# Performance work log

Measured on AMD Instinct MI355X. Metric: run time of the kernel, lower is better.

## Reference

```python
import jax, jax.numpy as jnp
import numpy as np

T, B, S = 8, 4, 2048
LAT, SYM, NC = 1024, 256, 512


def setup_inputs() -> dict:
    key = jax.random.key(0)
    ks = jax.random.split(key, 16)
    inp = {
        "token_state": jax.random.normal(ks[0], (B, S, LAT), jnp.float32),
        "bus_symbols": jax.random.normal(ks[1], (T, B, S, SYM), jnp.float32),
        "bus_indices": jax.random.randint(ks[2], (T, B, S), 0, NC),
        "bus_outputs": jax.random.normal(ks[3], (T, B, S, LAT), jnp.float32),
        "bus_mask": jnp.zeros((T,), jnp.bool_),
        # parameters (stored as (in, out) matrices)
        "Wq": jax.random.normal(ks[4], (SYM, 1), jnp.float32) / np.sqrt(SYM),
        "bq": jnp.zeros((1,), jnp.float32),
        "Wread": jax.random.normal(ks[5], (2 * LAT, LAT), jnp.float32) / np.sqrt(2 * LAT),
        "bread": jnp.zeros((LAT,), jnp.float32),
        "Wsym": jax.random.normal(ks[6], (LAT, SYM), jnp.float32) / np.sqrt(LAT),
        "bsym": jnp.zeros((SYM,), jnp.float32),
        "Wc1": jax.random.normal(ks[7], (LAT + SYM, LAT), jnp.float32) / np.sqrt(LAT + SYM),
        "bc1": jnp.zeros((LAT,), jnp.float32),
        "Wc2": jax.random.normal(ks[8], (LAT, LAT), jnp.float32) / np.sqrt(LAT),
        "bc2": jnp.zeros((LAT,), jnp.float32),
        "codebook": jax.random.normal(ks[9], (NC, SYM), jnp.float32),
    }
    return inp


def reference(token_state, bus_symbols, bus_indices, bus_outputs, bus_mask,
              Wq, bq, Wread, bread, Wsym, bsym, Wc1, bc1, Wc2, bc2, codebook):
    Tm, Bb, Ss, Dsym = bus_symbols.shape
    N = Bb * Ss
    syms = bus_symbols.reshape(Tm, N, Dsym)          # [T, N, SYM]
    outs = bus_outputs.reshape(Tm, N, -1)            # [T, N, LAT]

    # top-1 bus message routing
    relevance = (syms @ Wq + bq)[..., 0]             # [T, N]
    top_msg_idx = jnp.argmax(relevance, axis=0)      # [N]
    chosen = jnp.take_along_axis(outs, top_msg_idx[None, :, None], axis=0)[0]  # [N, LAT]
    bus_context = chosen.reshape(Bb, Ss, -1)

    z = jnp.concatenate([token_state, bus_context], axis=-1)
    z_read = z @ Wread + bread                       # [B, S, LAT]
    raw_symbol = z_read @ Wsym + bsym                # [B, S, SYM]

    # VQ: cdist argmin (squared distance has same argmin)
    flat = raw_symbol.reshape(-1, Dsym)              # [N, SYM]
    d2 = (jnp.sum(flat * flat, axis=1, keepdims=True)
          - 2.0 * flat @ codebook.T
          + jnp.sum(codebook * codebook, axis=1)[None, :])  # [N, NC]
    indices = jnp.argmin(d2, axis=-1)                # [N]
    quantized = codebook[indices].reshape(Bb, Ss, Dsym)

    h = jax.nn.relu(jnp.concatenate([z_read, quantized], axis=-1) @ Wc1 + bc1)
    node_output = h @ Wc2 + bc2 + token_state

    used_counts = jnp.zeros((Tm,), jnp.int32).at[top_msg_idx].add(1)
    keep_mask = used_counts == 0
    return node_output, quantized, indices.reshape(Bb, Ss), keep_mask
```

## Files before the change

### kernel.cpp

```cpp
#include <hip/hip_runtime.h>
#include <hip/hip_bf16.h>

#define DEVI __device__ __forceinline__

namespace {

constexpr int T_   = 8;
constexpr int NTOK = 8192;
constexpr int LAT  = 1024;
constexpr int SYM  = 256;
constexpr int NC   = 512;
constexpr float TAU = 0.6f;

typedef short short8 __attribute__((ext_vector_type(8)));
typedef float floatx4 __attribute__((ext_vector_type(4)));

DEVI unsigned short f2bf(float f){
  union { float f; unsigned u; } v; v.f = f;
  return (unsigned short)((v.u + 0x7fffu + ((v.u >> 16) & 1u)) >> 16);
}

DEVI void gload_lds16(const void* g, void* l){
  __builtin_amdgcn_global_load_lds((const __attribute__((address_space(1))) void*)g,
                                   (__attribute__((address_space(3))) void*)l, 16, 0, 0);
}

__global__ void routepack_k(const float* __restrict__ syms, const float* __restrict__ Wq,
                            const float* __restrict__ ts, const float* __restrict__ bus,
                            int* __restrict__ top, int* __restrict__ counts,
                            unsigned short* __restrict__ Az){
  int gt = blockIdx.x * blockDim.x + threadIdx.x;
  int wid = gt >> 6, lane = gt & 63;
  float4 wq = *(const float4*)(Wq + lane * 4);
  float best = -INFINITY; int bt = 0;
  for (int t = 0; t < T_; ++t){
    float4 s = *(const float4*)(syms + ((size_t)t * NTOK + wid) * SYM + lane * 4);
    float p = s.x*wq.x + s.y*wq.y + s.z*wq.z + s.w*wq.w;
    #pragma unroll
    for (int off = 32; off; off >>= 1) p += __shfl_down(p, off, 64);
    p = __shfl(p, 0, 64);
    if (p > best){ best = p; bt = t; }
  }
  if (lane == 0){ top[wid] = bt; atomicAdd(&counts[bt], 1); }
  const float* tsrow  = ts  + (size_t)wid * LAT;
  const float* busrow = bus + ((size_t)bt * NTOK + wid) * LAT;
  unsigned short* az  = Az + (size_t)wid * (2*LAT);
  #pragma unroll
  for (int i = 0; i < 4; ++i){
    int c = (i*64 + lane) * 4;
    float4 v = *(const float4*)(tsrow + c);
    ushort4 o; o.x = f2bf(v.x); o.y = f2bf(v.y); o.z = f2bf(v.z); o.w = f2bf(v.w);
    *(ushort4*)(az + c) = o;
    float4 w = *(const float4*)(busrow + c);
    ushort4 p2; p2.x = f2bf(w.x); p2.y = f2bf(w.y); p2.z = f2bf(w.z); p2.w = f2bf(w.w);
    *(ushort4*)(az + LAT + c) = p2;
  }
}

constexpr int MP_WFUSE = 128, MP_WCOMB = 384, MP_T32 = 4736, MP_CNORM = 4864;

DEVI void dev_wfuse(int tb, int tid, float* smem,
                    const float* __restrict__ Wsym, const float* __restrict__ cb,
                    unsigned short* __restrict__ WfuseT){
  float (*As)[68] = (float(*)[68])smem;
  float (*Bs)[68] = (float(*)[68])(smem + 544);
  const int bxm = tb & 15, byn = tb >> 4;
  const int m0 = bxm * 64, n0 = byn * 64;
  const int tx = tid & 15, ty = tid >> 4;
  float acc[4][4] = {};
  for (int k0 = 0; k0 < SYM; k0 += 8){
    if (tid < 128){
      int m = tid >> 1, kq = (tid & 1) * 4;
      float4 v = *(const float4*)(Wsym + (size_t)(m0+m) * SYM + k0 + kq);
      As[kq+0][m] = v.x; As[kq+1][m] = v.y; As[kq+2][m] = v.z; As[kq+3][m] = v.w;
    }
    {
      int n = tid >> 2, kk = (tid & 3) * 2;
      float2 v = *(const float2*)(cb + (size_t)(n0+n) * SYM + k0 + kk);
      Bs[kk+0][n] = v.x; Bs[kk+1][n] = v.y;
    }
    __syncthreads();
    #pragma unroll
    for (int k = 0; k < 8; ++k){
      float a[4], b[4];
      #pragma unroll
      for (int i = 0; i < 4; ++i) a[i] = As[k][ty*4 + i];
      #pragma unroll
      for (int j = 0; j < 4; ++j) b[j] = Bs[k][tx*4 + j];
      #pragma unroll
      for (int i = 0; i < 4; ++i)
        #pragma unroll
        for (int j = 0; j < 4; ++j) acc[i][j] += a[i] * b[j];
    }
    __syncthreads();
  }
  #pragma unroll
  for (int i = 0; i < 4; ++i)
    #pragma unroll
    for (int j = 0; j < 4; ++j)
      WfuseT[(size_t)(n0 + tx*4 + j) * LAT + m0 + ty*4 + i] = f2bf(acc[i][j]);
}

DEVI void dev_wcomb(int tb, int tid, float* smem,
                    const float* __restrict__ Wread, const float* __restrict__ Wsym,
                    float* __restrict__ Wcomb){
  float (*As)[68] = (float(*)[68])smem;
  float (*Bs)[68] = (float(*)[68])(smem + 544);
  const int bxm = tb & 63, byn = tb >> 6;
  const int m0 = bxm * 32, n0 = byn * 64;
  const int tx = tid & 15, ty = tid >> 4;
  float acc[2][4] = {};
  for (int k0 = 0; k0 < LAT; k0 += 8){
    if (tid < 64){
      int m = tid >> 1, kq = (tid & 1) * 4;
      float4 v = *(const float4*)(Wread + (size_t)(m0+m) * LAT + k0 + kq);
      As[kq+0][m] = v.x; As[kq+1][m] = v.y; As[kq+2][m] = v.z; As[kq+3][m] = v.w;
    }
    if (tid < 128){
      int k = tid >> 4, n4 = (tid & 15) * 4;
      *(float4*)&Bs[k][n4] = *(const float4*)(Wsym + (size_t)(k0+k) * SYM + n0 + n4);
    }
    __syncthreads();
    #pragma unroll
    for (int k = 0; k < 8; ++k){
      float a[2], b[4];
      #pragma unroll
      for (int i = 0; i < 2; ++i) a[i] = As[k][ty*2 + i];
      #pragma unroll
      for (int j = 0; j < 4; ++j) b[j] = Bs[k][tx*4 + j];
      #pragma unroll
      for (int i = 0; i < 2; ++i)
        #pragma unroll
        for (int j = 0; j < 4; ++j) acc[i][j] += a[i] * b[j];
    }
    __syncthreads();
  }
  #pragma unroll
  for (int i = 0; i < 2; ++i)
    #pragma unroll
    for (int j = 0; j < 4; ++j)
      Wcomb[(size_t)(m0 + ty*2 + i) * SYM + n0 + tx*4 + j] = acc[i][j];
}

DEVI void dev_t32(int t, int tid, float* smem,
                  const float* __restrict__ in, unsigned short* __restrict__ out,
                  int R, int C){
  float (*tile)[33] = (float(*)[33])smem;
  int bx = t % 32, by = t / 32;
  int r0 = by * 32, c0 = bx * 32;
  int tx = tid & 31, ty = tid >> 5;
  #pragma unroll
  for (int j = 0; j < 4; ++j)
    tile[ty + j*8][tx] = in[(size_t)(r0 + ty + j*8) * C + c0 + tx];
  __syncthreads();
  #pragma unroll
  for (int j = 0; j < 4; ++j)
    out[(size_t)(c0 + ty + j*8) * R + r0 + tx] = f2bf(tile[tx][ty + j*8]);
}

DEVI void dev_cnorm(int lb, int tid, const float* __restrict__ cb,
                    const float* __restrict__ bsym,
                    float* __restrict__ cnorm, float* __restrict__ svec){
  int wid = lb * 4 + (tid >> 6), lane = tid & 63;
  float4 v = *(const float4*)(cb + (size_t)wid * SYM + lane * 4);
  float4 b = *(const float4*)(bsym + lane * 4);
  float p = v.x*v.x + v.y*v.y + v.z*v.z + v.w*v.w;
  float q = v.x*(v.x-2.f*b.x) + v.y*(v.y-2.f*b.y) + v.z*(v.z-2.f*b.z) + v.w*(v.w-2.f*b.w);
  #pragma unroll
  for (int off = 32; off; off >>= 1){ p += __shfl_down(p, off, 64); q += __shfl_down(q, off, 64); }
  if (lane == 0){ cnorm[wid] = p; svec[wid] = q; }
}

DEVI void dev_rbias(int tid, const float* __restrict__ bread,
                    const float* __restrict__ Wsym, const float* __restrict__ bsym,
                    float* __restrict__ rb){
  float a0=0.f,a1=0.f,a2=0.f,a3=0.f;
  for (int k = 0; k < LAT; k += 4){
    a0 += bread[k+0] * Wsym[(size_t)(k+0) * SYM + tid];
    a1 += bread[k+1] * Wsym[(size_t)(k+1) * SYM + tid];
    a2 += bread[k+2] * Wsym[(size_t)(k+2) * SYM + tid];
    a3 += bread[k+3] * Wsym[(size_t)(k+3) * SYM + tid];
  }
  rb[tid] = bsym[tid] + ((a0+a1)+(a2+a3));
}

__global__ __launch_bounds__(256)
void megaprep_k(const float* __restrict__ Wsym, const float* __restrict__ cb,
                unsigned short* __restrict__ WfuseT,
                const float* __restrict__ Wread, float* __restrict__ Wcomb,
                unsigned short* __restrict__ WreadT,
                const float* __restrict__ Wc1, unsigned short* __restrict__ Wc1T,
                const float* __restrict__ Wc2, unsigned short* __restrict__ Wc2T,
                const float* __restrict__ bsym, float* __restrict__ cnorm,
                float* __restrict__ svec,
                const float* __restrict__ bread, float* __restrict__ rb){
  __shared__ float smem[1088];
  int b = blockIdx.x, tid = threadIdx.x;
  if (b < MP_WFUSE){
    dev_wfuse(b, tid, smem, Wsym, cb, WfuseT);
  } else if (b < MP_WCOMB){
    dev_wcomb(b - MP_WFUSE, tid, smem, Wread, Wsym, Wcomb);
  } else if (b < MP_T32){
    int t = b - MP_WCOMB;
    if (t < 2048)      dev_t32(t,        tid, smem, Wread, WreadT, 2*LAT, LAT);
    else if (t < 3328) dev_t32(t - 2048, tid, smem, Wc1,   Wc1T,   LAT+SYM, LAT);
    else               dev_t32(t - 3328, tid, smem, Wc2,   Wc2T,   LAT,  LAT);
  } else if (b < MP_CNORM){
    dev_cnorm(b - MP_T32, tid, cb, bsym, cnorm, svec);
  } else {
    dev_rbias(tid, bread, Wsym, bsym, rb);
  }
}

constexpr int A_PLAIN = 0, A_CAT = 1;
constexpr int EP_ZH = 0, EP_VQ = 1, EP_RELU = 2, EP_OUT = 3;

template<int ASRC, int EPI>
__global__ __launch_bounds__(256)
void mgemm(const unsigned short* __restrict__ A, const unsigned short* __restrict__ A2,
           const unsigned short* __restrict__ BT, const float* __restrict__ bias,
           const float* __restrict__ resid,
           unsigned short* __restrict__ Cb, float* __restrict__ Cf,
           int N, int K, int asplit)
{
  __shared__ unsigned short As[128*32];
  __shared__ unsigned short Bs[128*32];
  const int tid  = threadIdx.x;
  const int wave = tid >> 6, lane = tid & 63;
  const int wy = wave >> 1, wx = wave & 1;
  const int lq = lane >> 4, lr = lane & 15;

  const int nwg  = gridDim.x * gridDim.y;
  const int orig = blockIdx.y * gridDim.x + blockIdx.x;
  const int dec  = (orig & 7) * (nwg >> 3) + (orig >> 3);
  const int bx   = dec % gridDim.x, by = dec / gridDim.x;
  const int m0 = by * 128, n0 = bx * 128;

  floatx4 acc[4][4] = {};

  for (int k0 = 0; k0 < K; k0 += 32){
    #pragma unroll
    for (int c = 0; c < 2; ++c){
      int chunk = tid + c*256;
      int mrel = chunk >> 2, kc = (chunk & 3) * 8;
      int gk = k0 + kc;
      const unsigned short* srcA;
      if constexpr (ASRC == A_CAT){
        if (gk < asplit) srcA = A  + (size_t)(m0+mrel) * asplit + gk;
        else             srcA = A2 + (size_t)(m0+mrel) * (K-asplit) + (gk-asplit);
      } else {
        srcA = A + (size_t)(m0+mrel) * K + gk;
      }
      gload_lds16(srcA, &As[(c*256 + wave*64) * 8]);
      gload_lds16(BT + (size_t)(n0+mrel) * K + gk, &Bs[(c*256 + wave*64) * 8]);
    }
    __syncthreads();
    short8 af[4], bf[4];
    #pragma unroll
    for (int i = 0; i < 4; ++i){
      af[i] = *(const short8*)&As[(wy*64 + i*16 + lr)*32 + lq*8];
      bf[i] = *(const short8*)&Bs[(wx*64 + i*16 + lr)*32 + lq*8];
    }
    #pragma unroll
    for (int i = 0; i < 4; ++i)
      #pragma unroll
      for (int j = 0; j < 4; ++j)
        acc[i][j] = __builtin_amdgcn_mfma_f32_16x16x32_bf16(af[i], bf[j], acc[i][j], 0, 0, 0);
    __syncthreads();
  }

  #pragma unroll
  for (int i = 0; i < 4; ++i){
    #pragma unroll
    for (int j = 0; j < 4; ++j){
      int gn = n0 + wx*64 + j*16 + lr;
      #pragma unroll
      for (int r = 0; r < 4; ++r){
        int gm = m0 + wy*64 + i*16 + lq*4 + r;
        float v = acc[i][j][r];
        if constexpr (EPI == EP_ZH){
          Cb[(size_t)gm * N + gn] = f2bf(v + bias[gn]);
        } else if constexpr (EPI == EP_VQ){
          Cf[(size_t)gm * N + gn] = bias[gn] - 2.f * v;
        } else if constexpr (EPI == EP_RELU){
          float u = v + bias[gn];
          Cb[(size_t)gm * N + gn] = f2bf(u > 0.f ? u : 0.f);
        } else {
          Cf[(size_t)gm * N + gn] = v + bias[gn] + resid[(size_t)gm * N + gn];
        }
      }
    }
  }
}

__global__ void vq_k(const float* __restrict__ scores, const float* __restrict__ cb,
                     float* __restrict__ out_q, float* __restrict__ out_idx,
                     unsigned short* __restrict__ q_h,
                     int* __restrict__ rcount, int* __restrict__ rlist,
                     const int* __restrict__ counts, float* __restrict__ out_mask){
  if (blockIdx.x == 0 && threadIdx.x < T_)
    out_mask[threadIdx.x] = (counts[threadIdx.x] == 0) ? 1.0f : 0.0f;
  int gt = blockIdx.x * blockDim.x + threadIdx.x;
  int wid = gt >> 6, lane = gt & 63;
  if (wid >= NTOK) return;
  const float* row = scores + (size_t)wid * NC;
  float v1 = INFINITY, v2 = INFINITY; int i1 = 0x7fffffff;
  #pragma unroll
  for (int i = 0; i < NC/64; ++i){
    int c = i*64 + lane;
    float v = row[c];
    if (v < v1){ v2 = v1; v1 = v; i1 = c; } else v2 = fminf(v2, v);
  }
  #pragma unroll
  for (int off = 32; off; off >>= 1){
    float ov1 = __shfl_down(v1, off, 64);
    int   oi1 = __shfl_down(i1, off, 64);
    float ov2 = __shfl_down(v2, off, 64);
    float rest;
    if (ov1 < v1 || (ov1 == v1 && oi1 < i1)){ rest = v1; v1 = ov1; i1 = oi1; }
    else rest = ov1;
    v2 = fminf(fminf(v2, ov2), rest);
  }
  i1 = __shfl(i1, 0, 64);
  if (lane == 0){
    out_idx[wid] = (float)i1;
    if (__shfl(v2, 0, 64) - __shfl(v1, 0, 64) < TAU){
      int p = atomicAdd(rcount, 1); rlist[p] = wid;
    }
  }
  float4 cv = *(const float4*)(cb + (size_t)i1 * SYM + lane * 4);
  *(float4*)(out_q + (size_t)wid * SYM + lane * 4) = cv;
  ushort4 qh; qh.x = f2bf(cv.x); qh.y = f2bf(cv.y); qh.z = f2bf(cv.z); qh.w = f2bf(cv.w);
  *(ushort4*)(q_h + (size_t)wid * SYM + lane * 4) = qh;
}

constexpr int RT = 4;

__global__ __launch_bounds__(256)
void repair_k(const int* __restrict__ rcount, const int* __restrict__ rlist,
              const int* __restrict__ top,
              const float* __restrict__ ts, const float* __restrict__ bus,
              const float* __restrict__ Wcomb, const float* __restrict__ rb,
              const float* __restrict__ cb, const float* __restrict__ cnorm,
              float* __restrict__ out_q, float* __restrict__ out_idx,
              unsigned short* __restrict__ q_h){
  __shared__ float a[RT][2*LAT];
  __shared__ float raw[RT][SYM];
  __shared__ float pv[RT][4];
  __shared__ int   pi[RT][4];
  __shared__ int   fidx[RT];
  int tid = threadIdx.x;
  int lane = tid & 63, wave = tid >> 6;
  int cnt = *rcount;
  int nchunk = (cnt + RT - 1) / RT;
  for (int ch = blockIdx.x; ch < nchunk; ch += gridDim.x){
    int base = ch * RT;
    int nt = min(RT, cnt - base);
    for (int q = tid; q < nt * 512; q += 256){
      int t = q >> 9, c = (q & 511) * 4;
      int m = rlist[base + t];
      int tp = top[m];
      float4 v = (c < LAT) ? *(const float4*)(ts + (size_t)m * LAT + c)
                           : *(const float4*)(bus + ((size_t)tp * NTOK + m) * LAT + (c - LAT));
      *(float4*)&a[t][c] = v;
    }
    __syncthreads();
    float acc0[RT], acc1[RT], acc2[RT], acc3[RT];
    #pragma unroll
    for (int t = 0; t < RT; ++t){ acc0[t]=0.f; acc1[t]=0.f; acc2[t]=0.f; acc3[t]=0.f; }
    for (int k = 0; k < 2*LAT; k += 4){
      float w0 = Wcomb[(size_t)(k+0) * SYM + tid];
      float w1 = Wcomb[(size_t)(k+1) * SYM + tid];
      float w2 = Wcomb[(size_t)(k+2) * SYM + tid];
      float w3 = Wcomb[(size_t)(k+3) * SYM + tid];
      #pragma unroll
      for (int t = 0; t < RT; ++t){
        float4 av = *(const float4*)&a[t][k];
        acc0[t] += av.x * w0; acc1[t] += av.y * w1;
        acc2[t] += av.z * w2; acc3[t] += av.w * w3;
      }
    }
    #pragma unroll
    for (int t = 0; t < RT; ++t)
      raw[t][tid] = rb[tid] + ((acc0[t] + acc1[t]) + (acc2[t] + acc3[t]));
    __syncthreads();
    float bv[RT]; int bi[RT];
    #pragma unroll
    for (int t = 0; t < RT; ++t){ bv[t] = INFINITY; bi[t] = 0x7fffffff; }
    #pragma unroll
    for (int cc = 0; cc < 2; ++cc){
      int c = tid + cc * 256;
      const float* cr = cb + (size_t)c * SYM;
      float d[RT] = {};
      for (int j = 0; j < SYM; j += 4){
        float4 cv = *(const float4*)(cr + j);
        #pragma unroll
        for (int t = 0; t < RT; ++t){
          float4 rv4 = *(const float4*)&raw[t][j];
          d[t] += rv4.x*cv.x + rv4.y*cv.y + rv4.z*cv.z + rv4.w*cv.w;
        }
      }
      #pragma unroll
      for (int t = 0; t < RT; ++t){
        float s = cnorm[c] - 2.f * d[t];
        if (s < bv[t] || (s == bv[t] && c < bi[t])){ bv[t] = s; bi[t] = c; }
      }
    }
    #pragma unroll
    for (int t = 0; t < RT; ++t){
      float v = bv[t]; int i = bi[t];
      #pragma unroll
      for (int off = 32; off; off >>= 1){
        float ov = __shfl_down(v, off, 64);
        int   oi = __shfl_down(i, off, 64);
        if (ov < v || (ov == v && oi < i)){ v = ov; i = oi; }
      }
      if (lane == 0){ pv[t][wave] = v; pi[t][wave] = i; }
    }
    __syncthreads();
    if (tid < nt){
      float v = pv[tid][0]; int i = pi[tid][0];
      #pragma unroll
      for (int w = 1; w < 4; ++w){
        if (pv[tid][w] < v || (pv[tid][w] == v && pi[tid][w] < i)){ v = pv[tid][w]; i = pi[tid][w]; }
      }
      fidx[tid] = i;
      out_idx[rlist[base + tid]] = (float)i;
    }
    __syncthreads();
    for (int t = 0; t < nt; ++t){
      int m = rlist[base + t];
      int idx = fidx[t];
      float cvv = cb[(size_t)idx * SYM + tid];
      out_q[(size_t)m * SYM + tid] = cvv;
      q_h[(size_t)m * SYM + tid] = f2bf(cvv);
    }
    __syncthreads();
  }
}

}

extern "C" void kernel_launch(void* const* d_in, const int* in_sizes, int n_in,
                              void* d_out, int out_size, void* d_ws, size_t ws_size,
                              hipStream_t stream){
  const float* token_state = (const float*)d_in[0];
  const float* bus_symbols = (const float*)d_in[1];
  const float* bus_outputs = (const float*)d_in[3];
  const float* Wq    = (const float*)d_in[5];
  const float* Wread = (const float*)d_in[7];
  const float* bread = (const float*)d_in[8];
  const float* Wsym  = (const float*)d_in[9];
  const float* bsym  = (const float*)d_in[10];
  const float* Wc1   = (const float*)d_in[11];
  const float* bc1   = (const float*)d_in[12];
  const float* Wc2   = (const float*)d_in[13];
  const float* bc2   = (const float*)d_in[14];
  const float* codebook = (const float*)d_in[15];

  float* out_node = (float*)d_out;
  float* out_quant= out_node + (size_t)NTOK * LAT;
  float* out_idx  = out_quant + (size_t)NTOK * SYM;
  float* out_mask = out_idx + NTOK;

  char* W = (char*)d_ws; size_t off = 0;
  auto alloc = [&](size_t bytes)->char*{ char* p = W + off; off = (off + bytes + 255) & ~(size_t)255; return p; };
  int*   top     = (int*)alloc(NTOK*4);
  char*  zeroed  = alloc(256);
  int*   counts  = (int*)zeroed;
  int*   rcount  = (int*)(zeroed + 128);
  int*   rlist   = (int*)alloc(NTOK*4);
  float* cnorm   = (float*)alloc(NC*4);
  float* svec    = (float*)alloc(NC*4);
  float* rb      = (float*)alloc(SYM*4);
  float* Wcomb   = (float*)alloc((size_t)2*LAT*SYM*4);
  unsigned short* WreadT = (unsigned short*)alloc((size_t)LAT*2*LAT*2);
  unsigned short* Wc1T   = (unsigned short*)alloc((size_t)LAT*(LAT+SYM)*2);
  unsigned short* Wc2T   = (unsigned short*)alloc((size_t)LAT*LAT*2);
  unsigned short* WfuseT = (unsigned short*)alloc((size_t)NC*LAT*2);
  unsigned short* z_h    = (unsigned short*)alloc((size_t)NTOK*LAT*2);
  unsigned short* q_h    = (unsigned short*)alloc((size_t)NTOK*SYM*2);
  unsigned short* h_h    = (unsigned short*)alloc((size_t)NTOK*LAT*2);
  char* az_region        = alloc((size_t)NTOK*2*LAT*2);
  unsigned short* A_z    = (unsigned short*)az_region;
  float* scores          = (float*)az_region;

  hipMemsetAsync(zeroed, 0, 256, stream);

  routepack_k<<<NTOK/4, 256, 0, stream>>>(bus_symbols, Wq, token_state, bus_outputs,
                                          top, counts, A_z);
  megaprep_k<<<MP_CNORM + 1, 256, 0, stream>>>(
      Wsym, codebook, WfuseT, Wread, Wcomb, WreadT, Wc1, Wc1T, Wc2, Wc2T,
      bsym, cnorm, svec, bread, rb);

  mgemm<A_PLAIN, EP_ZH><<<dim3(LAT/128, NTOK/128), 256, 0, stream>>>(
      A_z, nullptr, WreadT, bread, nullptr, z_h, nullptr, LAT, 2*LAT, 0);
  mgemm<A_PLAIN, EP_VQ><<<dim3(NC/128, NTOK/128), 256, 0, stream>>>(
      z_h, nullptr, WfuseT, svec, nullptr, nullptr, scores, NC, LAT, 0);

  vq_k<<<NTOK/4, 256, 0, stream>>>(scores, codebook, out_quant, out_idx, q_h,
                                   rcount, rlist, counts, out_mask);
  repair_k<<<512, 256, 0, stream>>>(rcount, rlist, top, token_state, bus_outputs,
                                    Wcomb, rb, codebook, cnorm, out_quant, out_idx, q_h);

  mgemm<A_CAT, EP_RELU><<<dim3(LAT/128, NTOK/128), 256, 0, stream>>>(
      z_h, q_h, Wc1T, bc1, nullptr, h_h, nullptr, LAT, LAT+SYM, LAT);
  mgemm<A_PLAIN, EP_OUT><<<dim3(LAT/128, NTOK/128), 256, 0, stream>>>(
      h_h, nullptr, Wc2T, bc2, token_state, nullptr, out_node, LAT, LAT, 0);
}
```

Baseline: 797.9 us.

## Fuse VQ score GEMM with argmin and codebook gather into one kernel

Replaces the separate score GEMM, which wrote an fp32 NTOK x NC score matrix, and the vq_k argmin kernel with a single kernel. Each block computes 64 token rows against all 512 codewords and keeps top-2 values in registers, then gathers the chosen codewords. The per-token atomic count for the keep mask is replaced by a presence bitmask built in block 0, and the memset is replaced by zeroing rcount inside routepack_k. This removes the score matrix round trip and two launches, but the grid shrinks to 128 blocks with a 64-row tile, which may underfill the GPU, and block 0 carries extra mask work.

```diff
diff --git a/kernel.cpp b/kernel.cpp
--- a/kernel.cpp
+++ b/kernel.cpp
@@ -27,8 +27,9 @@
 
 __global__ void routepack_k(const float* __restrict__ syms, const float* __restrict__ Wq,
                             const float* __restrict__ ts, const float* __restrict__ bus,
-                            int* __restrict__ top, int* __restrict__ counts,
+                            int* __restrict__ top, int* __restrict__ rcount,
                             unsigned short* __restrict__ Az){
+  if (blockIdx.x == 0 && threadIdx.x == 0) *rcount = 0;
   int gt = blockIdx.x * blockDim.x + threadIdx.x;
   int wid = gt >> 6, lane = gt & 63;
   float4 wq = *(const float4*)(Wq + lane * 4);
@@ -41,7 +42,7 @@
     p = __shfl(p, 0, 64);
     if (p > best){ best = p; bt = t; }
   }
-  if (lane == 0){ top[wid] = bt; atomicAdd(&counts[bt], 1); }
+  if (lane == 0) top[wid] = bt;
   const float* tsrow  = ts  + (size_t)wid * LAT;
   const float* busrow = bus + ((size_t)bt * NTOK + wid) * LAT;
   unsigned short* az  = Az + (size_t)wid * (2*LAT);
@@ -213,7 +214,7 @@
 }
 
 constexpr int A_PLAIN = 0, A_CAT = 1;
-constexpr int EP_ZH = 0, EP_VQ = 1, EP_RELU = 2, EP_OUT = 3;
+constexpr int EP_ZH = 0, EP_RELU = 2, EP_OUT = 3;
 
 template<int ASRC, int EPI>
 __global__ __launch_bounds__(256)
@@ -280,8 +281,6 @@
         float v = acc[i][j][r];
         if constexpr (EPI == EP_ZH){
           Cb[(size_t)gm * N + gn] = f2bf(v + bias[gn]);
-        } else if constexpr (EPI == EP_VQ){
-          Cf[(size_t)gm * N + gn] = bias[gn] - 2.f * v;
         } else if constexpr (EPI == EP_RELU){
           float u = v + bias[gn];
           Cb[(size_t)gm * N + gn] = f2bf(u > 0.f ? u : 0.f);
@@ -293,45 +292,132 @@
   }
 }
 
-__global__ void vq_k(const float* __restrict__ scores, const float* __restrict__ cb,
-                     float* __restrict__ out_q, float* __restrict__ out_idx,
-                     unsigned short* __restrict__ q_h,
-                     int* __restrict__ rcount, int* __restrict__ rlist,
-                     const int* __restrict__ counts, float* __restrict__ out_mask){
-  if (blockIdx.x == 0 && threadIdx.x < T_)
-    out_mask[threadIdx.x] = (counts[threadIdx.x] == 0) ? 1.0f : 0.0f;
-  int gt = blockIdx.x * blockDim.x + threadIdx.x;
-  int wid = gt >> 6, lane = gt & 63;
-  if (wid >= NTOK) return;
-  const float* row = scores + (size_t)wid * NC;
-  float v1 = INFINITY, v2 = INFINITY; int i1 = 0x7fffffff;
-  #pragma unroll
-  for (int i = 0; i < NC/64; ++i){
-    int c = i*64 + lane;
-    float v = row[c];
-    if (v < v1){ v2 = v1; v1 = v; i1 = c; } else v2 = fminf(v2, v);
-  }
-  #pragma unroll
-  for (int off = 32; off; off >>= 1){
-    float ov1 = __shfl_down(v1, off, 64);
-    int   oi1 = __shfl_down(i1, off, 64);
-    float ov2 = __shfl_down(v2, off, 64);
-    float rest;
-    if (ov1 < v1 || (ov1 == v1 && oi1 < i1)){ rest = v1; v1 = ov1; i1 = oi1; }
-    else rest = ov1;
-    v2 = fminf(fminf(v2, ov2), rest);
-  }
-  i1 = __shfl(i1, 0, 64);
-  if (lane == 0){
-    out_idx[wid] = (float)i1;
-    if (__shfl(v2, 0, 64) - __shfl(v1, 0, 64) < TAU){
-      int p = atomicAdd(rcount, 1); rlist[p] = wid;
-    }
-  }
-  float4 cv = *(const float4*)(cb + (size_t)i1 * SYM + lane * 4);
-  *(float4*)(out_q + (size_t)wid * SYM + lane * 4) = cv;
-  ushort4 qh; qh.x = f2bf(cv.x); qh.y = f2bf(cv.y); qh.z = f2bf(cv.z); qh.w = f2bf(cv.w);
-  *(ushort4*)(q_h + (size_t)wid * SYM + lane * 4) = qh;
+__global__ __launch_bounds__(256)
+void vqgemm_k(const unsigned short* __restrict__ A ,
+              const unsigned short* __restrict__ BT ,
+              const float* __restrict__ svec, const float* __restrict__ cb,
+              const int* __restrict__ top,
+              float* __restrict__ out_q, float* __restrict__ out_idx,
+              unsigned short* __restrict__ q_h,
+              int* __restrict__ rcount, int* __restrict__ rlist,
+              float* __restrict__ out_mask)
+{
+  __shared__ unsigned short As[64*32];
+  __shared__ unsigned short Bs[128*32];
+  __shared__ float red_v1[64][2]; __shared__ int red_i1[64][2]; __shared__ float red_v2[64][2];
+  __shared__ int ridx[64];
+  __shared__ int presw[4];
+  const int tid = threadIdx.x;
+  const int wave = tid >> 6, lane = tid & 63;
+  const int wy = wave >> 1, wx = wave & 1;
+  const int lq = lane >> 4, lr = lane & 15;
+  const int nwg = gridDim.x;
+  const int orig = blockIdx.x;
+  const int blk = (orig & 7) * (nwg >> 3) + (orig >> 3);
+  const int m0 = blk * 64;
+
+  if (orig == 0){
+    int pres = 0;
+    for (int i = tid; i < NTOK; i += 256) pres |= 1 << top[i];
+    #pragma unroll
+    for (int off = 32; off; off >>= 1) pres |= __shfl_down(pres, off, 64);
+    if (lane == 0) presw[wave] = pres;
+    __syncthreads();
+    if (tid < T_){
+      int all = presw[0] | presw[1] | presw[2] | presw[3];
+      out_mask[tid] = ((all >> tid) & 1) ? 0.0f : 1.0f;
+    }
+    __syncthreads();
+  }
+
+  float t1v[8], t2v[8]; int t1i[8];
+  #pragma unroll
+  for (int q = 0; q < 8; ++q){ t1v[q] = INFINITY; t2v[q] = INFINITY; t1i[q] = 0x7fffffff; }
+
+  for (int nc = 0; nc < 4; ++nc){
+    const int n0c = nc * 128;
+    floatx4 acc[2][4] = {};
+    for (int k0 = 0; k0 < LAT; k0 += 32){
+      {
+        int mrel = tid >> 2, kc = (tid & 3) * 8;
+        gload_lds16(A + (size_t)(m0+mrel) * LAT + k0 + kc, &As[(wave*64) * 8]);
+      }
+      #pragma unroll
+      for (int c = 0; c < 2; ++c){
+        int chunk = tid + c*256;
+        int mrel = chunk >> 2, kc = (chunk & 3) * 8;
+        gload_lds16(BT + (size_t)(n0c+mrel) * LAT + k0 + kc, &Bs[(c*256 + wave*64) * 8]);
+      }
+      __syncthreads();
+      short8 af[2], bf[4];
+      #pragma unroll
+      for (int i = 0; i < 2; ++i)
+        af[i] = *(const short8*)&As[(wy*32 + i*16 + lr)*32 + lq*8];
+      #pragma unroll
+      for (int j = 0; j < 4; ++j)
+        bf[j] = *(const short8*)&Bs[(wx*64 + j*16 + lr)*32 + lq*8];
+      #pragma unroll
+      for (int i = 0; i < 2; ++i)
+        #pragma unroll
+        for (int j = 0; j < 4; ++j)
+          acc[i][j] = __builtin_amdgcn_mfma_f32_16x16x32_bf16(af[i], bf[j], acc[i][j], 0, 0, 0);
+      __syncthreads();
+    }
+    #pragma unroll
+    for (int j = 0; j < 4; ++j){
+      int col = n0c + wx*64 + j*16 + lr;
+      float sv = svec[col];
+      #pragma unroll
+      for (int i = 0; i < 2; ++i){
+        #pragma unroll
+        for (int r = 0; r < 4; ++r){
+          int q = i*4 + r;
+          float s = sv - 2.f * acc[i][j][r];
+          if (s < t1v[q]){ t2v[q] = t1v[q]; t1v[q] = s; t1i[q] = col; }
+          else t2v[q] = fminf(t2v[q], s);
+        }
+      }
+    }
+  }
+
+  #pragma unroll
+  for (int q = 0; q < 8; ++q){
+    float v1 = t1v[q]; int i1 = t1i[q]; float v2 = t2v[q];
+    #pragma unroll
+    for (int m = 8; m; m >>= 1){
+      float ov1 = __shfl_xor(v1, m, 64);
+      int   oi1 = __shfl_xor(i1, m, 64);
+      float ov2 = __shfl_xor(v2, m, 64);
+      if (ov1 < v1 || (ov1 == v1 && oi1 < i1)){ v2 = fminf(v1, ov2); v1 = ov1; i1 = oi1; }
+      else v2 = fminf(v2, ov1);
+    }
+    if (lr == 0){
+      int row = wy*32 + (q>>2)*16 + lq*4 + (q&3);
+      red_v1[row][wx] = v1; red_i1[row][wx] = i1; red_v2[row][wx] = v2;
+    }
+  }
+  __syncthreads();
+  if (tid < 64){
+    float v1 = red_v1[tid][0]; int i1 = red_i1[tid][0]; float v2 = red_v2[tid][0];
+    float ov1 = red_v1[tid][1]; int oi1 = red_i1[tid][1]; float ov2 = red_v2[tid][1];
+    if (ov1 < v1 || (ov1 == v1 && oi1 < i1)){ v2 = fminf(v1, ov2); v1 = ov1; i1 = oi1; }
+    else v2 = fminf(v2, ov1);
+    ridx[tid] = i1;
+    out_idx[m0 + tid] = (float)i1;
+    if (v2 - v1 < TAU){
+      int p = atomicAdd(rcount, 1); rlist[p] = m0 + tid;
+    }
+  }
+  __syncthreads();
+  #pragma unroll
+  for (int rr = 0; rr < 16; ++rr){
+    int row = rr*4 + wave;
+    int idx = ridx[row];
+    float4 cv = *(const float4*)(cb + (size_t)idx * SYM + lane * 4);
+    *(float4*)(out_q + (size_t)(m0+row) * SYM + lane * 4) = cv;
+    ushort4 qh; qh.x = f2bf(cv.x); qh.y = f2bf(cv.y); qh.z = f2bf(cv.z); qh.w = f2bf(cv.w);
+    *(ushort4*)(q_h + (size_t)(m0+row) * SYM + lane * 4) = qh;
+  }
 }
 
 constexpr int RT = 4;
@@ -466,9 +552,7 @@
   char* W = (char*)d_ws; size_t off = 0;
   auto alloc = [&](size_t bytes)->char*{ char* p = W + off; off = (off + bytes + 255) & ~(size_t)255; return p; };
   int*   top     = (int*)alloc(NTOK*4);
-  char*  zeroed  = alloc(256);
-  int*   counts  = (int*)zeroed;
-  int*   rcount  = (int*)(zeroed + 128);
+  int*   rcount  = (int*)alloc(256);
   int*   rlist   = (int*)alloc(NTOK*4);
   float* cnorm   = (float*)alloc(NC*4);
   float* svec    = (float*)alloc(NC*4);
@@ -481,25 +565,20 @@
   unsigned short* z_h    = (unsigned short*)alloc((size_t)NTOK*LAT*2);
   unsigned short* q_h    = (unsigned short*)alloc((size_t)NTOK*SYM*2);
   unsigned short* h_h    = (unsigned short*)alloc((size_t)NTOK*LAT*2);
-  char* az_region        = alloc((size_t)NTOK*2*LAT*2);
-  unsigned short* A_z    = (unsigned short*)az_region;
-  float* scores          = (float*)az_region;
-
-  hipMemsetAsync(zeroed, 0, 256, stream);
+  unsigned short* A_z    = (unsigned short*)alloc((size_t)NTOK*2*LAT*2);
 
   routepack_k<<<NTOK/4, 256, 0, stream>>>(bus_symbols, Wq, token_state, bus_outputs,
-                                          top, counts, A_z);
+                                          top, rcount, A_z);
   megaprep_k<<<MP_CNORM + 1, 256, 0, stream>>>(
       Wsym, codebook, WfuseT, Wread, Wcomb, WreadT, Wc1, Wc1T, Wc2, Wc2T,
       bsym, cnorm, svec, bread, rb);
 
   mgemm<A_PLAIN, EP_ZH><<<dim3(LAT/128, NTOK/128), 256, 0, stream>>>(
       A_z, nullptr, WreadT, bread, nullptr, z_h, nullptr, LAT, 2*LAT, 0);
-  mgemm<A_PLAIN, EP_VQ><<<dim3(NC/128, NTOK/128), 256, 0, stream>>>(
-      z_h, nullptr, WfuseT, svec, nullptr, nullptr, scores, NC, LAT, 0);
-
-  vq_k<<<NTOK/4, 256, 0, stream>>>(scores, codebook, out_quant, out_idx, q_h,
-                                   rcount, rlist, counts, out_mask);
+
+  vqgemm_k<<<NTOK/64, 256, 0, stream>>>(z_h, WfuseT, svec, codebook, top,
+                                        out_quant, out_idx, q_h, rcount, rlist, out_mask);
+
   repair_k<<<512, 256, 0, stream>>>(rcount, rlist, top, token_state, bus_outputs,
                                     Wcomb, rb, codebook, cnorm, out_quant, out_idx, q_h);
 
```

Result: faster. 778.8 us (-2.4%).
